# Performance work log

Measured on AMD Instinct MI355X. Metric: run time of the kernel, lower is better.

The kernel has to match this reference:

```python
import jax, jax.numpy as jnp
import numpy as np

B, EMB, H0, UP, M = 16, 128, 256, 512, 4
RADIUS, COEF = 60, 1.5


def affine_grid(theta, H, W):
    # theta [2,3]; normalized grid [H,W,2] (x=width coord, y=height coord), align_corners=False
    xs = (jnp.arange(W, dtype=jnp.float32) + 0.5) * (2.0 / W) - 1.0
    ys = (jnp.arange(H, dtype=jnp.float32) + 0.5) * (2.0 / H) - 1.0
    X, Y = jnp.meshgrid(xs, ys, indexing='xy')  # [H,W]
    gx = theta[0, 0] * X + theta[0, 1] * Y + theta[0, 2]
    gy = theta[1, 0] * X + theta[1, 1] * Y + theta[1, 2]
    return jnp.stack([gx, gy], axis=-1)


def grid_sample_bilinear(img, grid):
    # img [H,W], grid [Ho,Wo,2] normalized; zero padding, align_corners=False (PyTorch F.grid_sample semantics)
    H, W = img.shape
    x = ((grid[..., 0] + 1.0) * W - 1.0) * 0.5
    y = ((grid[..., 1] + 1.0) * H - 1.0) * 0.5
    x0f = jnp.floor(x)
    y0f = jnp.floor(y)
    wx = x - x0f
    wy = y - y0f

    def gather(yf, xf):
        valid = (xf >= 0) & (xf <= W - 1) & (yf >= 0) & (yf <= H - 1)
        yi = jnp.clip(yf, 0, H - 1).astype(jnp.int32)
        xi = jnp.clip(xf, 0, W - 1).astype(jnp.int32)
        return jnp.where(valid, img[yi, xi], 0.0)

    v00 = gather(y0f, x0f)
    v01 = gather(y0f, x0f + 1)
    v10 = gather(y0f + 1, x0f)
    v11 = gather(y0f + 1, x0f + 1)
    return v00 * (1 - wy) * (1 - wx) + v01 * (1 - wy) * wx + v10 * wy * (1 - wx) + v11 * wy * wx


def resize_bilinear(img, Ho, Wo):
    # PyTorch F.interpolate(mode='bilinear', align_corners=False)
    H, W = img.shape
    ys = jnp.clip((jnp.arange(Ho, dtype=jnp.float32) + 0.5) * (H / Ho) - 0.5, 0.0, H - 1.0)
    xs = jnp.clip((jnp.arange(Wo, dtype=jnp.float32) + 0.5) * (W / Wo) - 0.5, 0.0, W - 1.0)
    y0 = jnp.floor(ys).astype(jnp.int32)
    x0 = jnp.floor(xs).astype(jnp.int32)
    y1 = jnp.minimum(y0 + 1, H - 1)
    x1 = jnp.minimum(x0 + 1, W - 1)
    wy = (ys - y0)[:, None]
    wx = (xs - x0)[None, :]
    Ia = img[y0[:, None], x0[None, :]]
    Ib = img[y0[:, None], x1[None, :]]
    Ic = img[y1[:, None], x0[None, :]]
    Id = img[y1[:, None], x1[None, :]]
    return Ia * (1 - wy) * (1 - wx) + Ib * (1 - wy) * wx + Ic * wy * (1 - wx) + Id * wy * wx


# small disk mask at center of the 2*RADIUS crop (mask_function in source); dot_size = int(4*UP/200)
_DOT = int(4 * UP / 200)
_Yg, _Xg = np.ogrid[:2 * RADIUS, :2 * RADIUS]
SQ_MASK = jnp.asarray(((_Yg - RADIUS) ** 2 + (_Xg - RADIUS) ** 2) <= _DOT * _DOT)


def setup_inputs():
    key = jax.random.key(0)
    ks = jax.random.split(key, 6)
    x = jax.random.normal(ks[0], (B, 1, H0, H0), jnp.float32)
    k_out = jax.random.normal(ks[1], (B, EMB), jnp.float32)
    W_dec = jax.random.normal(ks[2], (EMB, H0 * H0), jnp.float32) * 0.05
    pert = 0.05 * jax.random.normal(ks[3], (B, 2, 2), jnp.float32)
    A1 = jnp.eye(2, dtype=jnp.float32)[None] + pert  # invertible scale/shear
    scaler_shear = jnp.concatenate([A1, jnp.zeros((B, 2, 1), jnp.float32)], axis=-1)
    ang = 0.2 * jax.random.normal(ks[4], (B,), jnp.float32)
    c, s = jnp.cos(ang), jnp.sin(ang)
    R = jnp.stack([jnp.stack([c, -s], -1), jnp.stack([s, c], -1)], -2)
    rotation = jnp.concatenate([R, jnp.zeros((B, 2, 1), jnp.float32)], axis=-1)
    adj_mask = 0.5 + jax.random.uniform(ks[5], (B,), jnp.float32)
    centers = [(160, 160), (160, 352), (352, 160), (352, 352)]
    Y, X = np.ogrid[:UP, :UP]
    masks = np.stack([(((Y - cy) ** 2 + (X - cx) ** 2) <= 24 ** 2).astype(np.float32) for cy, cx in centers])
    return {"x": x, "k_out": k_out, "W_dec": W_dec, "scaler_shear": scaler_shear,
            "rotation": rotation, "masks": jnp.asarray(masks), "adj_mask": adj_mask}


def _revise_one(cur, base_img, m, invt, adj):
    # per-sample: data-dependent COM, dynamic crop, adj divide (pare_reverse=True), inverse affine resample, paste
    new_img = base_img * m
    mean = jnp.sum(new_img) / jnp.maximum(jnp.sum(m), 1.0)
    sel = (m > 0) & (new_img > COEF * mean)
    w = jnp.where(sel, new_img, 0.0)
    tot = jnp.sum(w) + 1e-8
    r = jnp.arange(UP, dtype=jnp.float32)
    cx = jnp.sum(w * r[:, None]) / tot  # row coordinate
    cy = jnp.sum(w * r[None, :]) / tot  # col coordinate
    cxi = jnp.clip(jnp.round(cx), RADIUS, UP - RADIUS).astype(jnp.int32)
    cyi = jnp.clip(jnp.round(cy), RADIUS, UP - RADIUS).astype(jnp.int32)
    patch = jax.lax.dynamic_slice(cur, (cxi - RADIUS, cyi - RADIUS), (2 * RADIUS, 2 * RADIUS))
    patch = jnp.where(SQ_MASK, patch / adj, patch)
    re = grid_sample_bilinear(patch, affine_grid(invt, 2 * RADIUS, 2 * RADIUS))
    return jax.lax.dynamic_update_slice(cur, re, (cxi - RADIUS, cyi - RADIUS))


def _forward(x, k_out, W_dec, scaler_shear, rotation, masks, adj_mask):
    Bn = x.shape[0]
    bottom = jnp.broadcast_to(jnp.array([0.0, 0.0, 1.0], jnp.float32), (Bn, 1, 3))
    inv1 = jnp.linalg.inv(jnp.concatenate([scaler_shear, bottom], axis=1))[:, :2]
    inv2 = jnp.linalg.inv(jnp.concatenate([rotation, bottom], axis=1))[:, :2]
    base = jax.nn.relu(k_out @ W_dec).reshape(Bn, H0, H0)  # decoder
    base_inp = jax.vmap(lambda im: resize_bilinear(im, UP, UP))(base)
    grid1 = jax.vmap(lambda t: affine_grid(t, UP, UP))(inv1)
    grid2 = jax.vmap(lambda t: affine_grid(t, UP, UP))(inv2)
    pred_rot = jax.vmap(grid_sample_bilinear)(base_inp, grid2)
    pred_in = jax.vmap(grid_sample_bilinear)(pred_rot, grid1)
    # rotate masks through the same inverse affines, threshold at 0.5
    def rot_mask(mj):
        mb = jnp.broadcast_to(mj, (Bn, UP, UP))
        rm = jax.vmap(grid_sample_bilinear)(mb, grid2)
        rm = jax.vmap(grid_sample_bilinear)(rm, grid1)
        return (rm >= 0.5).astype(jnp.float32)
    rot_masks = jnp.stack([rot_mask(masks[j]) for j in range(masks.shape[0])])  # [M,B,UP,UP]
    img = pred_in
    for j in range(rot_masks.shape[0]):  # sequential over masks, vectorized over batch
        img = jax.vmap(_revise_one)(img, pred_in, rot_masks[j], inv1, adj_mask)
    return x, base_inp[:, None], img[:, None]


def reference(x, k_out, W_dec, scaler_shear, rotation, masks, adj_mask):
    return _forward(x, k_out, W_dec, scaler_shear, rotation, masks, adj_mask)
```

## Files before the change

### kernel.cpp

```cpp
#include <hip/hip_runtime.h>

#define BD 16
#define EMBD 128
#define H0D 256
#define UPD 512
#define RAD 60
#define PATCHD 120
#define COEFF 1.5f
#define NB 256
#define CHUNK 1024
#define SKIPR 32.0f


__device__ __forceinline__ float bsample(const float* __restrict__ img, int H, int W,
                                         float gx, float gy) {
    float xs = ((gx + 1.f) * (float)W - 1.f) * 0.5f;
    float ys = ((gy + 1.f) * (float)H - 1.f) * 0.5f;
    float x0f = floorf(xs), y0f = floorf(ys);
    float wx = xs - x0f, wy = ys - y0f;
    int x0 = (int)x0f, y0 = (int)y0f;
    bool vx0 = (x0 >= 0) && (x0 <= W - 1);
    bool vx1 = (x0 + 1 >= 0) && (x0 + 1 <= W - 1);
    bool vy0 = (y0 >= 0) && (y0 <= H - 1);
    bool vy1 = (y0 + 1 >= 0) && (y0 + 1 <= H - 1);
    int xi0 = min(max(x0, 0), W - 1);
    int xi1 = min(max(x0 + 1, 0), W - 1);
    int yi0 = min(max(y0, 0), H - 1);
    int yi1 = min(max(y0 + 1, 0), H - 1);
    float v00 = (vy0 && vx0) ? img[yi0 * W + xi0] : 0.f;
    float v01 = (vy0 && vx1) ? img[yi0 * W + xi1] : 0.f;
    float v10 = (vy1 && vx0) ? img[yi1 * W + xi0] : 0.f;
    float v11 = (vy1 && vx1) ? img[yi1 * W + xi1] : 0.f;
    return v00 * (1.f - wy) * (1.f - wx) + v01 * (1.f - wy) * wx +
           v10 * wy * (1.f - wx) + v11 * wy * wx;
}


__global__ void k_inv(const float* __restrict__ ss, const float* __restrict__ rot,
                      float* __restrict__ invbuf) {
    int b = threadIdx.x;
    if (b < BD) {
        {
            const float* A = ss + b * 6;
            float a = A[0], bb = A[1], c = A[3], d = A[4];
            float det = a * d - bb * c;
            float* o = invbuf + b * 6;
            o[0] = d / det; o[1] = -bb / det; o[2] = 0.f;
            o[3] = -c / det; o[4] = a / det; o[5] = 0.f;
        }
        {
            const float* A = rot + b * 6;
            float a = A[0], bb = A[1], c = A[3], d = A[4];
            float det = a * d - bb * c;
            float* o = invbuf + 96 + b * 6;
            o[0] = d / det; o[1] = -bb / det; o[2] = 0.f;
            o[3] = -c / det; o[4] = a / det; o[5] = 0.f;
        }
    }
}

__global__ __launch_bounds__(256) void k_gemm(const float* __restrict__ kout,
                                              const float* __restrict__ Wd,
                                              float* __restrict__ base) {
    __shared__ float sk[BD * EMBD];
    int t = threadIdx.x;
    for (int i = t; i < BD * EMBD; i += 256) sk[i] = kout[i];
    __syncthreads();
    int n = blockIdx.x * 256 + t;
    float acc[BD];
#pragma unroll
    for (int b = 0; b < BD; b++) acc[b] = 0.f;
    for (int e = 0; e < EMBD; e++) {
        float w = Wd[(size_t)e * (H0D * H0D) + n];
#pragma unroll
        for (int b = 0; b < BD; b++) acc[b] += sk[b * EMBD + e] * w;
    }
#pragma unroll
    for (int b = 0; b < BD; b++)
        base[(size_t)b * (H0D * H0D) + n] = fmaxf(acc[b], 0.f);
}

__global__ __launch_bounds__(256) void k_resize(const float* __restrict__ base,
                                                float* __restrict__ out) {
    int g = blockIdx.x;
    int b = g & (BD - 1);
    int blk = g >> 4;
    int t = threadIdx.x;
    const float* img = base + (size_t)b * (H0D * H0D);
    float* ob = out + (size_t)b * (UPD * UPD);
    for (int k = 0; k < CHUNK / 256; k++) {
        int p = blk * CHUNK + k * 256 + t;
        int yo = p >> 9, xo = p & 511;
        float ysf = fminf(fmaxf(((float)yo + 0.5f) * 0.5f - 0.5f, 0.f), 255.f);
        float xsf = fminf(fmaxf(((float)xo + 0.5f) * 0.5f - 0.5f, 0.f), 255.f);
        int y0 = (int)floorf(ysf), x0 = (int)floorf(xsf);
        int y1 = min(y0 + 1, H0D - 1), x1 = min(x0 + 1, H0D - 1);
        float wy = ysf - (float)y0, wx = xsf - (float)x0;
        float Ia = img[y0 * H0D + x0], Ib = img[y0 * H0D + x1];
        float Ic = img[y1 * H0D + x0], Id = img[y1 * H0D + x1];
        ob[p] = Ia * (1.f - wy) * (1.f - wx) + Ib * (1.f - wy) * wx +
                Ic * wy * (1.f - wx) + Id * wy * wx;
    }
}

__global__ __launch_bounds__(256) void k_sample(const float* __restrict__ in,
                                                const float* __restrict__ theta,
                                                float* __restrict__ out) {
    int g = blockIdx.x;
    int b = g & (BD - 1);
    int blk = g >> 4;
    int t = threadIdx.x;
    const float* th = theta + b * 6;
    float a0 = th[0], a1 = th[1], a2 = th[2];
    float a3 = th[3], a4 = th[4], a5 = th[5];
    const float* img = in + (size_t)b * (UPD * UPD);
    float* ob = out + (size_t)b * (UPD * UPD);
    for (int k = 0; k < CHUNK / 256; k++) {
        int p = blk * CHUNK + k * 256 + t;
        int yo = p >> 9, xo = p & 511;
        float X = ((float)xo + 0.5f) * (2.f / UPD) - 1.f;
        float Y = ((float)yo + 0.5f) * (2.f / UPD) - 1.f;
        float gx = a0 * X + a1 * Y + a2;
        float gy = a3 * X + a4 * Y + a5;
        ob[p] = bsample(img, UPD, UPD, gx, gy);
    }
}

__global__ void k_pack(const float* __restrict__ masks, float4* __restrict__ packed) {
    int p = blockIdx.x * blockDim.x + threadIdx.x;
    if (p >= UPD * UPD) return;
    float4 v;
    v.x = masks[p];
    v.y = masks[(size_t)(UPD * UPD) + p];
    v.z = masks[(size_t)2 * (UPD * UPD) + p];
    v.w = masks[(size_t)3 * (UPD * UPD) + p];
    packed[p] = v;
}

__global__ __launch_bounds__(256) void k_predmask(
        const float* __restrict__ pred_rot, const float4* __restrict__ packed,
        const float* __restrict__ invbuf, float* __restrict__ out_img,
        uchar4* __restrict__ rm, float* __restrict__ part1,
        unsigned int* __restrict__ flags) {
    int g = blockIdx.x;
    int b = g & (BD - 1);
    int blk = g >> 4;
    int t = threadIdx.x;
    const float* th1 = invbuf + b * 6;
    const float* th2 = invbuf + 96 + b * 6;
    float a10 = th1[0], a11 = th1[1], a12 = th1[2];
    float a13 = th1[3], a14 = th1[4], a15 = th1[5];
    float a20 = th2[0], a21 = th2[1], a22 = th2[2];
    float a23 = th2[3], a24 = th2[4], a25 = th2[5];

    __shared__ unsigned int sflag;
    if (t == 0) {
        const float crow[4] = {160.f, 160.f, 352.f, 352.f};
        const float ccol[4] = {160.f, 352.f, 160.f, 352.f};
        unsigned int f = 0;
        int r0 = blk * 2;
        for (int rr = 0; rr < 2; rr++) {
            float Y = ((float)(r0 + rr) + 0.5f) * (2.f / UPD) - 1.f;
            float X0 = 0.5f * (2.f / UPD) - 1.f;
            float X1 = 511.5f * (2.f / UPD) - 1.f;
            float gx0 = a10 * X0 + a11 * Y + a12, gy0 = a13 * X0 + a14 * Y + a15;
            float gx1 = a10 * X1 + a11 * Y + a12, gy1 = a13 * X1 + a14 * Y + a15;
            float c0 = 256.f * (a20 * gx0 + a21 * gy0 + a22) + 255.5f;
            float w0 = 256.f * (a23 * gx0 + a24 * gy0 + a25) + 255.5f;
            float c1 = 256.f * (a20 * gx1 + a21 * gy1 + a22) + 255.5f;
            float w1 = 256.f * (a23 * gx1 + a24 * gy1 + a25) + 255.5f;
            float vx = c1 - c0, vy = w1 - w0;
            float vv = fmaxf(vx * vx + vy * vy, 1e-12f);
            for (int j = 0; j < 4; j++) {
                float ux = c0 - ccol[j], uy = w0 - crow[j];
                float tt = fminf(fmaxf(-(ux * vx + uy * vy) / vv, 0.f), 1.f);
                float dx = ux + tt * vx, dy = uy + tt * vy;
                if (dx * dx + dy * dy <= SKIPR * SKIPR) f |= (1u << j);
            }
        }
        sflag = f;
        flags[b * NB + blk] = f;
        if (f == 0) {
#pragma unroll
            for (int j = 0; j < 4; j++) {
                part1[((size_t)(j * BD + b) * NB + blk) * 2 + 0] = 0.f;
                part1[((size_t)(j * BD + b) * NB + blk) * 2 + 1] = 0.f;
            }
        }
    }
    __syncthreads();
    unsigned int f = sflag;

    const float* pr = pred_rot + (size_t)b * (UPD * UPD);
    float* oi = out_img + (size_t)b * (UPD * UPD);
    uchar4* rmb = rm + (size_t)b * (UPD * UPD);
    float s_new[4] = {0.f, 0.f, 0.f, 0.f};
    float s_m[4] = {0.f, 0.f, 0.f, 0.f};
    int base = blk * CHUNK;
    for (int k = 0; k < CHUNK / 256; k++) {
        int p = base + k * 256 + t;
        int yo = p >> 9, xo = p & 511;
        float X = ((float)xo + 0.5f) * (2.f / UPD) - 1.f;
        float Y = ((float)yo + 0.5f) * (2.f / UPD) - 1.f;
        float gx = a10 * X + a11 * Y + a12;
        float gy = a13 * X + a14 * Y + a15;
        float xs = ((gx + 1.f) * (float)UPD - 1.f) * 0.5f;
        float ys = ((gy + 1.f) * (float)UPD - 1.f) * 0.5f;
        float x0f = floorf(xs), y0f = floorf(ys);
        float wx = xs - x0f, wy = ys - y0f;
        int x0 = (int)x0f, y0 = (int)y0f;
        bool pact = false;
        if (f) {
            float cxp = 256.f * (a20 * gx + a21 * gy + a22) + 255.5f;
            float cwp = 256.f * (a23 * gx + a24 * gy + a25) + 255.5f;
            const float crow[4] = {160.f, 160.f, 352.f, 352.f};
            const float ccol[4] = {160.f, 352.f, 160.f, 352.f};
#pragma unroll
            for (int j = 0; j < 4; j++) {
                float dx = cxp - ccol[j], dy = cwp - crow[j];
                if (dx * dx + dy * dy <= SKIPR * SKIPR) pact = true;
            }
        }
        float piv = 0.f;
        float m0 = 0.f, m1 = 0.f, m2 = 0.f, m3 = 0.f;
#pragma unroll
        for (int q = 0; q < 4; q++) {
            int qy = y0 + (q >> 1), qx = x0 + (q & 1);
            bool qv = (qx >= 0) && (qx < UPD) && (qy >= 0) && (qy < UPD);
            float fy = (q >> 1) ? wy : (1.f - wy);
            float fx = (q & 1) ? wx : (1.f - wx);
            if (qv) {
                piv += pr[qy * UPD + qx] * fy * fx;
                if (pact) {
                    float Xq = ((float)qx + 0.5f) * (2.f / UPD) - 1.f;
                    float Yq = ((float)qy + 0.5f) * (2.f / UPD) - 1.f;
                    float g2x = a20 * Xq + a21 * Yq + a22;
                    float g2y = a23 * Xq + a24 * Yq + a25;
                    float xs2 = ((g2x + 1.f) * (float)UPD - 1.f) * 0.5f;
                    float ys2 = ((g2y + 1.f) * (float)UPD - 1.f) * 0.5f;
                    float x0f2 = floorf(xs2), y0f2 = floorf(ys2);
                    float wx2 = xs2 - x0f2, wy2 = ys2 - y0f2;
                    int x02 = (int)x0f2, y02 = (int)y0f2;
                    bool vx0 = (x02 >= 0) && (x02 <= UPD - 1);
                    bool vx1 = (x02 + 1 >= 0) && (x02 + 1 <= UPD - 1);
                    bool vy0 = (y02 >= 0) && (y02 <= UPD - 1);
                    bool vy1 = (y02 + 1 >= 0) && (y02 + 1 <= UPD - 1);
                    int xi0 = min(max(x02, 0), UPD - 1);
                    int xi1 = min(max(x02 + 1, 0), UPD - 1);
                    int yi0 = min(max(y02, 0), UPD - 1);
                    int yi1 = min(max(y02 + 1, 0), UPD - 1);
                    float4 c00 = packed[yi0 * UPD + xi0];
                    float4 c01 = packed[yi0 * UPD + xi1];
                    float4 c10 = packed[yi1 * UPD + xi0];
                    float4 c11 = packed[yi1 * UPD + xi1];
                    const float* f00 = (const float*)&c00;
                    const float* f01 = (const float*)&c01;
                    const float* f10 = (const float*)&c10;
                    const float* f11 = (const float*)&c11;
                    float rq[4];
#pragma unroll
                    for (int j = 0; j < 4; j++) {
                        float v00 = (vy0 && vx0) ? f00[j] : 0.f;
                        float v01 = (vy0 && vx1) ? f01[j] : 0.f;
                        float v10 = (vy1 && vx0) ? f10[j] : 0.f;
                        float v11 = (vy1 && vx1) ? f11[j] : 0.f;
                        rq[j] = v00 * (1.f - wy2) * (1.f - wx2) +
                                v01 * (1.f - wy2) * wx2 +
                                v10 * wy2 * (1.f - wx2) + v11 * wy2 * wx2;
                    }
                    m0 += rq[0] * fy * fx;
                    m1 += rq[1] * fy * fx;
                    m2 += rq[2] * fy * fx;
                    m3 += rq[3] * fy * fx;
                }
            }
        }
        oi[p] = piv;
        if (f) {
            uchar4 rmv;
            unsigned char* rmc = (unsigned char*)&rmv;
            float mj[4] = {m0, m1, m2, m3};
#pragma unroll
            for (int j = 0; j < 4; j++) {
                float mm = (mj[j] >= 0.5f) ? 1.f : 0.f;
                rmc[j] = (unsigned char)mm;
                s_new[j] += piv * mm;
                s_m[j] += mm;
            }
            rmb[p] = rmv;
        }
    }
    if (f) {
        __shared__ float r1[256], r2[256];
        for (int j = 0; j < 4; j++) {
            r1[t] = s_new[j];
            r2[t] = s_m[j];
            __syncthreads();
            for (int s = 128; s > 0; s >>= 1) {
                if (t < s) { r1[t] += r1[t + s]; r2[t] += r2[t + s]; }
                __syncthreads();
            }
            if (t == 0) {
                part1[((size_t)(j * BD + b) * NB + blk) * 2 + 0] = r1[0];
                part1[((size_t)(j * BD + b) * NB + blk) * 2 + 1] = r2[0];
            }
            __syncthreads();
        }
    }
}

__global__ __launch_bounds__(256) void k_maskB(
        const float* __restrict__ pred_in, const uchar4* __restrict__ rm,
        const float* __restrict__ part1, float* __restrict__ part2,
        const unsigned int* __restrict__ flags) {
    int g = blockIdx.x;
    int b = g & (BD - 1);
    int blk = g >> 4;
    int t = threadIdx.x;
    unsigned int flag = flags[b * NB + blk];
    if (flag == 0) {
        if (t == 0) {
#pragma unroll
            for (int j = 0; j < 4; j++) {
                float* o = part2 + ((size_t)(j * BD + b) * NB + blk) * 4;
                o[0] = 0.f; o[1] = 0.f; o[2] = 0.f;
            }
        }
        return;
    }
    __shared__ float r1[256], r2[256], r3[256];
    float thr[4];
    for (int j = 0; j < 4; j++) {
        r1[t] = part1[((size_t)(j * BD + b) * NB + t) * 2 + 0];
        r2[t] = part1[((size_t)(j * BD + b) * NB + t) * 2 + 1];
        __syncthreads();
        for (int s = 128; s > 0; s >>= 1) {
            if (t < s) { r1[t] += r1[t + s]; r2[t] += r2[t + s]; }
            __syncthreads();
        }
        thr[j] = COEFF * (r1[0] / fmaxf(r2[0], 1.f));
        __syncthreads();
    }
    float tot[4] = {0.f, 0.f, 0.f, 0.f};
    float sx[4] = {0.f, 0.f, 0.f, 0.f};
    float sy[4] = {0.f, 0.f, 0.f, 0.f};
    int base = blk * CHUNK;
    const float* pi = pred_in + (size_t)b * (UPD * UPD);
    const uchar4* rmb = rm + (size_t)b * (UPD * UPD);
    for (int k = 0; k < CHUNK / 256; k++) {
        int p = base + k * 256 + t;
        uchar4 mm4 = rmb[p];
        unsigned int mmbits;
        __builtin_memcpy(&mmbits, &mm4, 4);
        if (mmbits == 0) continue;
        float piv = pi[p];
        float fi = (float)(p >> 9), fj = (float)(p & 511);
        const unsigned char* mmc = (const unsigned char*)&mm4;
#pragma unroll
        for (int j = 0; j < 4; j++) {
            float mm = (float)mmc[j];
            float ni = piv * mm;
            bool sel = (mm > 0.f) && (ni > thr[j]);
            float w = sel ? ni : 0.f;
            tot[j] += w;
            sx[j] += w * fi;
            sy[j] += w * fj;
        }
    }
    for (int j = 0; j < 4; j++) {
        r1[t] = tot[j]; r2[t] = sx[j]; r3[t] = sy[j];
        __syncthreads();
        for (int s = 128; s > 0; s >>= 1) {
            if (t < s) { r1[t] += r1[t + s]; r2[t] += r2[t + s]; r3[t] += r3[t + s]; }
            __syncthreads();
        }
        if (t == 0) {
            float* o = part2 + ((size_t)(j * BD + b) * NB + blk) * 4;
            o[0] = r1[0]; o[1] = r2[0]; o[2] = r3[0];
        }
        __syncthreads();
    }
}

#define CENT_REDUCE(part2, b, t, cs)                                             \
    {                                                                            \
        __shared__ float r1[256], r2[256], r3[256];                              \
        for (int j = 0; j < 4; j++) {                                            \
            if (t < 256) {                                                       \
                const float* pp2 = part2 + ((size_t)(j * BD + b) * NB + t) * 4;  \
                r1[t] = pp2[0]; r2[t] = pp2[1]; r3[t] = pp2[2];                  \
            }                                                                    \
            __syncthreads();                                                     \
            for (int s = 128; s > 0; s >>= 1) {                                  \
                if (t < s) {                                                     \
                    r1[t] += r1[t + s]; r2[t] += r2[t + s]; r3[t] += r3[t + s];  \
                }                                                                \
                __syncthreads();                                                 \
            }                                                                    \
            if (t == 0) {                                                        \
                float tot_ = r1[0] + 1e-8f;                                      \
                float cx_ = r2[0] / tot_;                                        \
                float cy_ = r3[0] / tot_;                                        \
                cs[j * 2 + 0] =                                                  \
                    (int)fminf(fmaxf(rintf(cx_), (float)RAD), (float)(UPD - RAD));\
                cs[j * 2 + 1] =                                                  \
                    (int)fminf(fmaxf(rintf(cy_), (float)RAD), (float)(UPD - RAD));\
            }                                                                    \
            __syncthreads();                                                     \
        }                                                                        \
        if (t == 0) {                                                            \
            int ov_ = 0;                                                         \
            for (int a_ = 0; a_ < 4; a_++)                                       \
                for (int c_ = a_ + 1; c_ < 4; c_++) {                            \
                    int dr = cs[a_ * 2] - cs[c_ * 2];                            \
                    int dc = cs[a_ * 2 + 1] - cs[c_ * 2 + 1];                    \
                    if (dr < 0) dr = -dr;                                        \
                    if (dc < 0) dc = -dc;                                        \
                    if (dr < 2 * RAD && dc < 2 * RAD) ov_ = 1;                   \
                }                                                                \
            cs[8] = ov_;                                                         \
        }                                                                        \
        __syncthreads();                                                         \
    }

__global__ __launch_bounds__(1024) void k_rev1(
        const float* __restrict__ part2, const float* __restrict__ invbuf,
        const float* __restrict__ adj, float* __restrict__ img,
        float* __restrict__ patchOut) {
    int b = blockIdx.x >> 2;
    int jown = blockIdx.x & 3;
    int t = threadIdx.x;
    __shared__ int cs[9];
    CENT_REDUCE(part2, b, t, cs);
    const float* th = invbuf + b * 6;
    float th0 = th[0], th1v = th[1], th2v = th[2];
    float th3v = th[3], th4v = th[4], th5v = th[5];
    float a = adj[b];
    float* im = img + (size_t)b * (UPD * UPD);
    if (cs[8]) {
        if (jown != 0) return;
        __shared__ float patch[PATCHD * PATCHD];
        for (int j = 0; j < 4; j++) {
            int cxi = cs[j * 2 + 0], cyi = cs[j * 2 + 1];
            for (int p = t; p < PATCHD * PATCHD; p += 1024) {
                int i = p / PATCHD, jj = p - i * PATCHD;
                float v = im[(cxi - RAD + i) * UPD + (cyi - RAD + jj)];
                int di = i - RAD, dj = jj - RAD;
                if (di * di + dj * dj <= 100) v /= a;
                patch[p] = v;
            }
            __syncthreads();
            for (int p = t; p < PATCHD * PATCHD; p += 1024) {
                int i = p / PATCHD, jj = p - i * PATCHD;
                float X = ((float)jj + 0.5f) * (2.f / PATCHD) - 1.f;
                float Y = ((float)i + 0.5f) * (2.f / PATCHD) - 1.f;
                float gx = th0 * X + th1v * Y + th2v;
                float gy = th3v * X + th4v * Y + th5v;
                float v = bsample(patch, PATCHD, PATCHD, gx, gy);
                im[(cxi - RAD + i) * UPD + (cyi - RAD + jj)] = v;
            }
            __syncthreads();
        }
        return;
    }
    int cxi = cs[jown * 2 + 0], cyi = cs[jown * 2 + 1];
    float* po = patchOut + (size_t)(b * 4 + jown) * (PATCHD * PATCHD);
    for (int p = t; p < PATCHD * PATCHD; p += 1024) {
        int i = p / PATCHD, jj = p - i * PATCHD;
        float X = ((float)jj + 0.5f) * (2.f / PATCHD) - 1.f;
        float Y = ((float)i + 0.5f) * (2.f / PATCHD) - 1.f;
        float gx = th0 * X + th1v * Y + th2v;
        float gy = th3v * X + th4v * Y + th5v;
        float xs = ((gx + 1.f) * (float)PATCHD - 1.f) * 0.5f;
        float ys = ((gy + 1.f) * (float)PATCHD - 1.f) * 0.5f;
        float x0f = floorf(xs), y0f = floorf(ys);
        float wx = xs - x0f, wy = ys - y0f;
        int x0 = (int)x0f, y0 = (int)y0f;
        float vq[4];
#pragma unroll
        for (int q = 0; q < 4; q++) {
            int qy = y0 + (q >> 1), qx = x0 + (q & 1);
            bool qv = (qx >= 0) && (qx <= PATCHD - 1) && (qy >= 0) && (qy <= PATCHD - 1);
            float v = 0.f;
            if (qv) {
                v = im[(cxi - RAD + qy) * UPD + (cyi - RAD + qx)];
                int di = qy - RAD, dj = qx - RAD;
                if (di * di + dj * dj <= 100) v /= a;
            }
            vq[q] = v;
        }
        po[p] = vq[0] * (1.f - wy) * (1.f - wx) + vq[1] * (1.f - wy) * wx +
                vq[2] * wy * (1.f - wx) + vq[3] * wy * wx;
    }
}

__global__ __launch_bounds__(1024) void k_rev2(
        const float* __restrict__ part2, const float* __restrict__ patchOut,
        float* __restrict__ img) {
    int b = blockIdx.x >> 2;
    int j = blockIdx.x & 3;
    int t = threadIdx.x;
    __shared__ int cs[9];
    CENT_REDUCE(part2, b, t, cs);
    if (cs[8]) return;
    int cxi = cs[j * 2 + 0], cyi = cs[j * 2 + 1];
    float* im = img + (size_t)b * (UPD * UPD);
    const float* po = patchOut + (size_t)(b * 4 + j) * (PATCHD * PATCHD);
    for (int p = t; p < PATCHD * PATCHD; p += 1024) {
        int i = p / PATCHD, jj = p - i * PATCHD;
        im[(cxi - RAD + i) * UPD + (cyi - RAD + jj)] = po[p];
    }
}


extern "C" void kernel_launch(void* const* d_in, const int* in_sizes, int n_in,
                              void* d_out, int out_size, void* d_ws, size_t ws_size,
                              hipStream_t stream) {
    const float* x = (const float*)d_in[0];
    const float* k_out = (const float*)d_in[1];
    const float* W_dec = (const float*)d_in[2];
    const float* ss = (const float*)d_in[3];
    const float* rot = (const float*)d_in[4];
    const float* masks = (const float*)d_in[5];
    const float* adj = (const float*)d_in[6];

    float* out = (float*)d_out;
    const size_t NX = (size_t)BD * H0D * H0D;
    const size_t P = (size_t)BD * UPD * UPD;
    float* out_x = out;
    float* out_base = out + NX;
    float* out_img = out + NX + P;

    float* ws = (float*)d_ws;
    float* slotR = ws;
    uchar4* rm = (uchar4*)(ws + P);
    float* slotC = ws + 2 * P;
    float* patchOut = slotC;
    float* invbuf = ws + 2 * P + P / 4;
    float* part1 = invbuf + 192;
    float* part2 = part1 + 4 * BD * NB * 2;
    unsigned int* flags = (unsigned int*)(part2 + 4 * BD * NB * 4);
    float4* packed = (float4*)((float*)(flags + BD * NB));

    hipMemcpyAsync(out_x, x, NX * sizeof(float), hipMemcpyDeviceToDevice, stream);

    k_inv<<<1, 64, 0, stream>>>(ss, rot, invbuf);
    float* inv2 = invbuf + 96;

    k_pack<<<(UPD * UPD) / 256, 256, 0, stream>>>(masks, packed);
    k_gemm<<<(H0D * H0D) / 256, 256, 0, stream>>>(k_out, W_dec, slotC);
    k_resize<<<BD * NB, 256, 0, stream>>>(slotC, out_base);

    k_sample<<<BD * NB, 256, 0, stream>>>(out_base, inv2, slotR);
    k_predmask<<<BD * NB, 256, 0, stream>>>(slotR, packed, invbuf, out_img, rm,
                                            part1, flags);
    k_maskB<<<BD * NB, 256, 0, stream>>>(out_img, rm, part1, part2, flags);
    k_rev1<<<BD * 4, 1024, 0, stream>>>(part2, invbuf, adj, out_img, patchOut);
    k_rev2<<<BD * 4, 1024, 0, stream>>>(part2, patchOut, out_img);
}
```

Baseline: 129.6 us.

## Fuse small setup kernels, vectorize sampling stores, merge revise passes

The affine inversion moves into an extra block of the GEMM kernel. Mask packing and the input copy are folded into the resize kernel as extra blocks, which replaces the separate memcpy and pack launches. Resize and affine sampling now have each thread produce four consecutive pixels and write them with one float4 store. The two-pass revise (write to a scratch patch buffer, then copy back) becomes a single kernel that stages each patch in shared memory. Together these cut launch count and global scratch traffic, at the cost of less coalesced gather reads per thread.

Result: faster. 114.1 us (-12.0%).

```diff
diff --git a/kernel.cpp b/kernel.cpp
--- a/kernel.cpp
+++ b/kernel.cpp
@@ -36,32 +36,34 @@
 }
 
 
-__global__ void k_inv(const float* __restrict__ ss, const float* __restrict__ rot,
-                      float* __restrict__ invbuf) {
-    int b = threadIdx.x;
-    if (b < BD) {
-        {
-            const float* A = ss + b * 6;
-            float a = A[0], bb = A[1], c = A[3], d = A[4];
-            float det = a * d - bb * c;
-            float* o = invbuf + b * 6;
-            o[0] = d / det; o[1] = -bb / det; o[2] = 0.f;
-            o[3] = -c / det; o[4] = a / det; o[5] = 0.f;
-        }
-        {
-            const float* A = rot + b * 6;
-            float a = A[0], bb = A[1], c = A[3], d = A[4];
-            float det = a * d - bb * c;
-            float* o = invbuf + 96 + b * 6;
-            o[0] = d / det; o[1] = -bb / det; o[2] = 0.f;
-            o[3] = -c / det; o[4] = a / det; o[5] = 0.f;
-        }
-    }
-}
-
 __global__ __launch_bounds__(256) void k_gemm(const float* __restrict__ kout,
                                               const float* __restrict__ Wd,
-                                              float* __restrict__ base) {
+                                              float* __restrict__ base,
+                                              const float* __restrict__ ss,
+                                              const float* __restrict__ rot,
+                                              float* __restrict__ invbuf) {
+    if (blockIdx.x == 256) {
+        int b = threadIdx.x;
+        if (b < BD) {
+            {
+                const float* A = ss + b * 6;
+                float a = A[0], bb = A[1], c = A[3], d = A[4];
+                float det = a * d - bb * c;
+                float* o = invbuf + b * 6;
+                o[0] = d / det; o[1] = -bb / det; o[2] = 0.f;
+                o[3] = -c / det; o[4] = a / det; o[5] = 0.f;
+            }
+            {
+                const float* A = rot + b * 6;
+                float a = A[0], bb = A[1], c = A[3], d = A[4];
+                float det = a * d - bb * c;
+                float* o = invbuf + 96 + b * 6;
+                o[0] = d / det; o[1] = -bb / det; o[2] = 0.f;
+                o[3] = -c / det; o[4] = a / det; o[5] = 0.f;
+            }
+        }
+        return;
+    }
     __shared__ float sk[BD * EMBD];
     int t = threadIdx.x;
     for (int i = t; i < BD * EMBD; i += 256) sk[i] = kout[i];
@@ -80,26 +82,46 @@
         base[(size_t)b * (H0D * H0D) + n] = fmaxf(acc[b], 0.f);
 }
 
-__global__ __launch_bounds__(256) void k_resize(const float* __restrict__ base,
-                                                float* __restrict__ out) {
+__global__ __launch_bounds__(256) void k_stage(
+        const float* __restrict__ base, float* __restrict__ out_base,
+        const float* __restrict__ masks, float4* __restrict__ packed,
+        const float* __restrict__ x, float* __restrict__ out_x) {
     int g = blockIdx.x;
-    int b = g & (BD - 1);
-    int blk = g >> 4;
     int t = threadIdx.x;
-    const float* img = base + (size_t)b * (H0D * H0D);
-    float* ob = out + (size_t)b * (UPD * UPD);
-    for (int k = 0; k < CHUNK / 256; k++) {
-        int p = blk * CHUNK + k * 256 + t;
-        int yo = p >> 9, xo = p & 511;
-        float ysf = fminf(fmaxf(((float)yo + 0.5f) * 0.5f - 0.5f, 0.f), 255.f);
-        float xsf = fminf(fmaxf(((float)xo + 0.5f) * 0.5f - 0.5f, 0.f), 255.f);
-        int y0 = (int)floorf(ysf), x0 = (int)floorf(xsf);
-        int y1 = min(y0 + 1, H0D - 1), x1 = min(x0 + 1, H0D - 1);
-        float wy = ysf - (float)y0, wx = xsf - (float)x0;
-        float Ia = img[y0 * H0D + x0], Ib = img[y0 * H0D + x1];
-        float Ic = img[y1 * H0D + x0], Id = img[y1 * H0D + x1];
-        ob[p] = Ia * (1.f - wy) * (1.f - wx) + Ib * (1.f - wy) * wx +
-                Ic * wy * (1.f - wx) + Id * wy * wx;
+    if (g < BD * NB) {
+        int b = g & (BD - 1);
+        int blk = g >> 4;
+        const float* img = base + (size_t)b * (H0D * H0D);
+        float* ob = out_base + (size_t)b * (UPD * UPD);
+        int p0 = blk * CHUNK + t * 4;
+        float4 o;
+        float* op = (float*)&o;
+#pragma unroll
+        for (int u = 0; u < 4; u++) {
+            int p = p0 + u;
+            int yo = p >> 9, xo = p & 511;
+            float ysf = fminf(fmaxf(((float)yo + 0.5f) * 0.5f - 0.5f, 0.f), 255.f);
+            float xsf = fminf(fmaxf(((float)xo + 0.5f) * 0.5f - 0.5f, 0.f), 255.f);
+            int y0 = (int)floorf(ysf), x0 = (int)floorf(xsf);
+            int y1 = min(y0 + 1, H0D - 1), x1 = min(x0 + 1, H0D - 1);
+            float wy = ysf - (float)y0, wx = xsf - (float)x0;
+            float Ia = img[y0 * H0D + x0], Ib = img[y0 * H0D + x1];
+            float Ic = img[y1 * H0D + x0], Id = img[y1 * H0D + x1];
+            op[u] = Ia * (1.f - wy) * (1.f - wx) + Ib * (1.f - wy) * wx +
+                    Ic * wy * (1.f - wx) + Id * wy * wx;
+        }
+        *(float4*)(ob + p0) = o;
+    } else if (g < BD * NB + 1024) {
+        int p = (g - BD * NB) * 256 + t;
+        float4 v;
+        v.x = masks[p];
+        v.y = masks[(size_t)(UPD * UPD) + p];
+        v.z = masks[(size_t)2 * (UPD * UPD) + p];
+        v.w = masks[(size_t)3 * (UPD * UPD) + p];
+        packed[p] = v;
+    } else {
+        int idx = (g - BD * NB - 1024) * 256 + t;
+        ((float4*)out_x)[idx] = ((const float4*)x)[idx];
     }
 }
 
@@ -115,26 +137,20 @@
     float a3 = th[3], a4 = th[4], a5 = th[5];
     const float* img = in + (size_t)b * (UPD * UPD);
     float* ob = out + (size_t)b * (UPD * UPD);
-    for (int k = 0; k < CHUNK / 256; k++) {
-        int p = blk * CHUNK + k * 256 + t;
+    int p0 = blk * CHUNK + t * 4;
+    float4 o;
+    float* op = (float*)&o;
+#pragma unroll
+    for (int u = 0; u < 4; u++) {
+        int p = p0 + u;
         int yo = p >> 9, xo = p & 511;
         float X = ((float)xo + 0.5f) * (2.f / UPD) - 1.f;
         float Y = ((float)yo + 0.5f) * (2.f / UPD) - 1.f;
         float gx = a0 * X + a1 * Y + a2;
         float gy = a3 * X + a4 * Y + a5;
-        ob[p] = bsample(img, UPD, UPD, gx, gy);
-    }
-}
-
-__global__ void k_pack(const float* __restrict__ masks, float4* __restrict__ packed) {
-    int p = blockIdx.x * blockDim.x + threadIdx.x;
-    if (p >= UPD * UPD) return;
-    float4 v;
-    v.x = masks[p];
-    v.y = masks[(size_t)(UPD * UPD) + p];
-    v.z = masks[(size_t)2 * (UPD * UPD) + p];
-    v.w = masks[(size_t)3 * (UPD * UPD) + p];
-    packed[p] = v;
+        op[u] = bsample(img, UPD, UPD, gx, gy);
+    }
+    *(float4*)(ob + p0) = o;
 }
 
 __global__ __launch_bounds__(256) void k_predmask(
@@ -423,10 +439,9 @@
         __syncthreads();                                                         \
     }
 
-__global__ __launch_bounds__(1024) void k_rev1(
+__global__ __launch_bounds__(1024) void k_revise(
         const float* __restrict__ part2, const float* __restrict__ invbuf,
-        const float* __restrict__ adj, float* __restrict__ img,
-        float* __restrict__ patchOut) {
+        const float* __restrict__ adj, float* __restrict__ img) {
     int b = blockIdx.x >> 2;
     int jown = blockIdx.x & 3;
     int t = threadIdx.x;
@@ -437,78 +452,32 @@
     float th3v = th[3], th4v = th[4], th5v = th[5];
     float a = adj[b];
     float* im = img + (size_t)b * (UPD * UPD);
+    __shared__ float patch[PATCHD * PATCHD];
+    int jlo = jown, jhi = jown + 1;
     if (cs[8]) {
         if (jown != 0) return;
-        __shared__ float patch[PATCHD * PATCHD];
-        for (int j = 0; j < 4; j++) {
-            int cxi = cs[j * 2 + 0], cyi = cs[j * 2 + 1];
-            for (int p = t; p < PATCHD * PATCHD; p += 1024) {
-                int i = p / PATCHD, jj = p - i * PATCHD;
-                float v = im[(cxi - RAD + i) * UPD + (cyi - RAD + jj)];
-                int di = i - RAD, dj = jj - RAD;
-                if (di * di + dj * dj <= 100) v /= a;
-                patch[p] = v;
-            }
-            __syncthreads();
-            for (int p = t; p < PATCHD * PATCHD; p += 1024) {
-                int i = p / PATCHD, jj = p - i * PATCHD;
-                float X = ((float)jj + 0.5f) * (2.f / PATCHD) - 1.f;
-                float Y = ((float)i + 0.5f) * (2.f / PATCHD) - 1.f;
-                float gx = th0 * X + th1v * Y + th2v;
-                float gy = th3v * X + th4v * Y + th5v;
-                float v = bsample(patch, PATCHD, PATCHD, gx, gy);
-                im[(cxi - RAD + i) * UPD + (cyi - RAD + jj)] = v;
-            }
-            __syncthreads();
-        }
-        return;
-    }
-    int cxi = cs[jown * 2 + 0], cyi = cs[jown * 2 + 1];
-    float* po = patchOut + (size_t)(b * 4 + jown) * (PATCHD * PATCHD);
-    for (int p = t; p < PATCHD * PATCHD; p += 1024) {
-        int i = p / PATCHD, jj = p - i * PATCHD;
-        float X = ((float)jj + 0.5f) * (2.f / PATCHD) - 1.f;
-        float Y = ((float)i + 0.5f) * (2.f / PATCHD) - 1.f;
-        float gx = th0 * X + th1v * Y + th2v;
-        float gy = th3v * X + th4v * Y + th5v;
-        float xs = ((gx + 1.f) * (float)PATCHD - 1.f) * 0.5f;
-        float ys = ((gy + 1.f) * (float)PATCHD - 1.f) * 0.5f;
-        float x0f = floorf(xs), y0f = floorf(ys);
-        float wx = xs - x0f, wy = ys - y0f;
-        int x0 = (int)x0f, y0 = (int)y0f;
-        float vq[4];
-#pragma unroll
-        for (int q = 0; q < 4; q++) {
-            int qy = y0 + (q >> 1), qx = x0 + (q & 1);
-            bool qv = (qx >= 0) && (qx <= PATCHD - 1) && (qy >= 0) && (qy <= PATCHD - 1);
-            float v = 0.f;
-            if (qv) {
-                v = im[(cxi - RAD + qy) * UPD + (cyi - RAD + qx)];
-                int di = qy - RAD, dj = qx - RAD;
-                if (di * di + dj * dj <= 100) v /= a;
-            }
-            vq[q] = v;
-        }
-        po[p] = vq[0] * (1.f - wy) * (1.f - wx) + vq[1] * (1.f - wy) * wx +
-                vq[2] * wy * (1.f - wx) + vq[3] * wy * wx;
-    }
-}
-
-__global__ __launch_bounds__(1024) void k_rev2(
-        const float* __restrict__ part2, const float* __restrict__ patchOut,
-        float* __restrict__ img) {
-    int b = blockIdx.x >> 2;
-    int j = blockIdx.x & 3;
-    int t = threadIdx.x;
-    __shared__ int cs[9];
-    CENT_REDUCE(part2, b, t, cs);
-    if (cs[8]) return;
-    int cxi = cs[j * 2 + 0], cyi = cs[j * 2 + 1];
-    float* im = img + (size_t)b * (UPD * UPD);
-    const float* po = patchOut + (size_t)(b * 4 + j) * (PATCHD * PATCHD);
-    for (int p = t; p < PATCHD * PATCHD; p += 1024) {
-        int i = p / PATCHD, jj = p - i * PATCHD;
-        im[(cxi - RAD + i) * UPD + (cyi - RAD + jj)] = po[p];
+        jlo = 0; jhi = 4;
+    }
+    for (int j = jlo; j < jhi; j++) {
+        int cxi = cs[j * 2 + 0], cyi = cs[j * 2 + 1];
+        for (int p = t; p < PATCHD * PATCHD; p += 1024) {
+            int i = p / PATCHD, jj = p - i * PATCHD;
+            float v = im[(cxi - RAD + i) * UPD + (cyi - RAD + jj)];
+            int di = i - RAD, dj = jj - RAD;
+            if (di * di + dj * dj <= 100) v /= a;
+            patch[p] = v;
+        }
+        __syncthreads();
+        for (int p = t; p < PATCHD * PATCHD; p += 1024) {
+            int i = p / PATCHD, jj = p - i * PATCHD;
+            float X = ((float)jj + 0.5f) * (2.f / PATCHD) - 1.f;
+            float Y = ((float)i + 0.5f) * (2.f / PATCHD) - 1.f;
+            float gx = th0 * X + th1v * Y + th2v;
+            float gy = th3v * X + th4v * Y + th5v;
+            float v = bsample(patch, PATCHD, PATCHD, gx, gy);
+            im[(cxi - RAD + i) * UPD + (cyi - RAD + jj)] = v;
+        }
+        __syncthreads();
     }
 }
 
@@ -535,26 +504,20 @@
     float* slotR = ws;
     uchar4* rm = (uchar4*)(ws + P);
     float* slotC = ws + 2 * P;
-    float* patchOut = slotC;
     float* invbuf = ws + 2 * P + P / 4;
     float* part1 = invbuf + 192;
     float* part2 = part1 + 4 * BD * NB * 2;
     unsigned int* flags = (unsigned int*)(part2 + 4 * BD * NB * 4);
     float4* packed = (float4*)((float*)(flags + BD * NB));
 
-    hipMemcpyAsync(out_x, x, NX * sizeof(float), hipMemcpyDeviceToDevice, stream);
-
-    k_inv<<<1, 64, 0, stream>>>(ss, rot, invbuf);
     float* inv2 = invbuf + 96;
 
-    k_pack<<<(UPD * UPD) / 256, 256, 0, stream>>>(masks, packed);
-    k_gemm<<<(H0D * H0D) / 256, 256, 0, stream>>>(k_out, W_dec, slotC);
-    k_resize<<<BD * NB, 256, 0, stream>>>(slotC, out_base);
-
+    k_gemm<<<257, 256, 0, stream>>>(k_out, W_dec, slotC, ss, rot, invbuf);
+    k_stage<<<BD * NB + 2048, 256, 0, stream>>>(slotC, out_base, masks, packed,
+                                                x, out_x);
     k_sample<<<BD * NB, 256, 0, stream>>>(out_base, inv2, slotR);
     k_predmask<<<BD * NB, 256, 0, stream>>>(slotR, packed, invbuf, out_img, rm,
                                             part1, flags);
     k_maskB<<<BD * NB, 256, 0, stream>>>(out_img, rm, part1, part2, flags);
-    k_rev1<<<BD * 4, 1024, 0, stream>>>(part2, invbuf, adj, out_img, patchOut);
-    k_rev2<<<BD * 4, 1024, 0, stream>>>(part2, patchOut, out_img);
-}
+    k_revise<<<BD * 4, 1024, 0, stream>>>(part2, invbuf, adj, out_img);
+}
```
